# Performance work log

Measured on AMD Instinct MI355X. Metric: run time of the kernel, lower is better.

The kernel has to match this reference:

```python
import jax, jax.numpy as jnp
import numpy as np

HEADS = 4  # from init_kwargs

def setup_inputs() -> dict:
    key = jax.random.key(0)
    ks = jax.random.split(key, 11)
    B, N, T, E = 1, 16, 2048, 64
    D = E // HEADS
    return {
        "value": jax.random.normal(ks[0], (B, N, T, E), jnp.float32),
        "key":   jax.random.normal(ks[1], (B, N, T, E), jnp.float32),
        "query": jax.random.normal(ks[2], (B, N, T, E), jnp.float32),
        "Wq": jax.random.normal(ks[3], (D, D), jnp.float32) / np.sqrt(D),
        "bq": jax.random.normal(ks[4], (D,), jnp.float32) * 0.01,
        "Wk": jax.random.normal(ks[5], (D, D), jnp.float32) / np.sqrt(D),
        "bk": jax.random.normal(ks[6], (D,), jnp.float32) * 0.01,
        "Wv": jax.random.normal(ks[7], (D, D), jnp.float32) / np.sqrt(D),
        "bv": jax.random.normal(ks[8], (D,), jnp.float32) * 0.01,
        "Wfc": jax.random.normal(ks[9], (E, E), jnp.float32) / np.sqrt(E),
        "bfc": jax.random.normal(ks[10], (E,), jnp.float32) * 0.01,
    }

def reference(value, key, query, Wq, bq, Wk, bk, Wv, bv, Wfc, bfc):
    B, N, T, E = query.shape
    H = HEADS
    D = E // H
    # split heads: [B,N,T,H,D]
    q = query.reshape(B, N, T, H, D) @ Wq + bq
    k = key.reshape(B, N, T, H, D) @ Wk + bk
    v = value.reshape(B, N, T, H, D) @ Wv + bv
    # full score tensor [B,N,Tq,Tk,H]
    scores = jnp.einsum('bnqhd,bnkhd->bnqkh', q, k)
    # NOTE: original softmaxes over dim=2, i.e. the QUERY axis (faithful to source)
    attn = jax.nn.softmax(scores / jnp.float32(E) ** 0.5, axis=2)
    out = jnp.einsum('bnqkh,bnkhd->bnqhd', attn, v).reshape(B, N, T, E)
    return out @ Wfc + bfc
```

## Files before the change

kernel.cpp:

```cpp
#include <hip/hip_runtime.h>

#define N_ 16
#define T_ 2048
#define E_ 64
#define H_ 4
#define D_ 16
#define NH_ 64
#define SEXP_ 0.18033688f

typedef __attribute__((ext_vector_type(4))) _Float16 h4;
typedef __attribute__((ext_vector_type(8))) _Float16 h8;
typedef __attribute__((ext_vector_type(2))) __fp16 g2;
typedef __attribute__((ext_vector_type(4))) float f4;

#if __has_builtin(__builtin_amdgcn_exp2f)
__device__ inline float fast_exp2(float x) { return __builtin_amdgcn_exp2f(x); }
#else
__device__ inline float fast_exp2(float x) {
    float r; asm("v_exp_f32 %0, %1" : "=v"(r) : "v"(x)); return r;
}
#endif

#if __has_builtin(__builtin_amdgcn_rcpf)
__device__ inline float fast_rcp(float x) { return __builtin_amdgcn_rcpf(x); }
#else
__device__ inline float fast_rcp(float x) {
    float r; asm("v_rcp_f32 %0, %1" : "=v"(r) : "v"(x)); return r;
}
#endif

__device__ inline h4 pack4_f16(float a, float b, float c, float d) {
    union { g2 g[2]; h4 h; } u;
    u.g[0] = __builtin_amdgcn_cvt_pkrtz(a, b);
    u.g[1] = __builtin_amdgcn_cvt_pkrtz(c, d);
    return u.h;
}

__global__ __launch_bounds__(256) void proj_kernel(
    const float* __restrict__ xq, const float* __restrict__ Wq, const float* __restrict__ bq,
    const float* __restrict__ xk, const float* __restrict__ Wk, const float* __restrict__ bk,
    const float* __restrict__ xv, const float* __restrict__ Wv, const float* __restrict__ bv,
    const float* __restrict__ Wfc,
    _Float16* __restrict__ Qh, _Float16* __restrict__ Kh, _Float16* __restrict__ Vt,
    _Float16* __restrict__ Wt)
{
    int tid = threadIdx.x;
    int y = blockIdx.y;
    if (y == 3) {
        if (blockIdx.x < 16) {
            int k = blockIdx.x * 4 + (tid >> 6);
            int e = tid & 63;
            Wt[e * 64 + k] = (_Float16)Wfc[k * 64 + e];
        }
        return;
    }
    const float* x = (y == 0) ? xq : (y == 1) ? xk : xv;
    const float* W = (y == 0) ? Wq : (y == 1) ? Wk : Wv;
    const float* b = (y == 0) ? bq : (y == 1) ? bk : bv;
    const float sc = (y == 0) ? SEXP_ : 1.0f;

    __shared__ float Wl[D_ * D_];
    __shared__ float bl[D_];
    Wl[tid] = W[tid];
    if (tid < D_) bl[tid] = b[tid];
    __syncthreads();

    int r = blockIdx.x * 256 + tid;
    int h, t, n;
    if (y == 2) {
        t = r & (T_ - 1);
        h = (r >> 11) & (H_ - 1);
        n = r >> 13;
    } else {
        h = r & (H_ - 1);
        t = (r >> 2) & (T_ - 1);
        n = r >> 13;
    }

    const float4* xp4 = reinterpret_cast<const float4*>(
        x + ((size_t)(n * T_ + t) * E_ + h * D_));
    float xv_[D_];
#pragma unroll
    for (int i = 0; i < 4; i++) {
        float4 v = xp4[i];
        xv_[4*i] = v.x; xv_[4*i+1] = v.y; xv_[4*i+2] = v.z; xv_[4*i+3] = v.w;
    }
    float acc[D_];
#pragma unroll
    for (int i = 0; i < D_; i++) acc[i] = bl[i];
#pragma unroll
    for (int j = 0; j < D_; j++) {
        float xj = xv_[j];
#pragma unroll
        for (int i = 0; i < D_; i++) acc[i] = fmaf(xj, Wl[j * D_ + i], acc[i]);
    }
    if (y == 2) {
        _Float16* vb = Vt + (size_t)(n * H_ + h) * D_ * T_ + t;
#pragma unroll
        for (int d = 0; d < D_; d++) vb[(size_t)d * T_] = (_Float16)acc[d];
    } else {
        _Float16 ob[16];
#pragma unroll
        for (int i = 0; i < D_; i++) ob[i] = (_Float16)(acc[i] * sc);
        _Float16* o = (y == 0) ? Qh : Kh;
        uint4* dst = reinterpret_cast<uint4*>(o + (size_t)((n * H_ + h) * T_ + t) * D_);
        dst[0] = reinterpret_cast<uint4*>(ob)[0];
        dst[1] = reinterpret_cast<uint4*>(ob)[1];
    }
}

#define S_PHASE(PD) do {                                                      \
    lp = (f4){0.f, 0.f, 0.f, 0.f};                                            \
    _Pragma("unroll")                                                         \
    for (int j = 0; j < 8; j++) {                                             \
        h4 bj = *reinterpret_cast<const h4*>(QsW + (j * 16 + row) * 20 + quad * 4); \
        f4 s = __builtin_amdgcn_mfma_f32_16x16x16f16(a, bj, z4, 0, 0, 0);     \
        float e0 = fast_exp2(s[0]), e1 = fast_exp2(s[1]);                     \
        float e2 = fast_exp2(s[2]), e3 = fast_exp2(s[3]);                     \
        lp[0] += e0; lp[1] += e1; lp[2] += e2; lp[3] += e3;                   \
        PD[j] = pack4_f16(e0, e1, e2, e3);                                    \
    }                                                                         \
} while (0)

#define SWZ_STEP(M)                                                           \
    lp[0] += __int_as_float(__builtin_amdgcn_ds_swizzle(__float_as_int(lp[0]), M)); \
    lp[1] += __int_as_float(__builtin_amdgcn_ds_swizzle(__float_as_int(lp[1]), M)); \
    lp[2] += __int_as_float(__builtin_amdgcn_ds_swizzle(__float_as_int(lp[2]), M)); \
    lp[3] += __int_as_float(__builtin_amdgcn_ds_swizzle(__float_as_int(lp[3]), M));

#define REDUCE(BDST) do {                                                     \
    SWZ_STEP(0x041F) SWZ_STEP(0x081F) SWZ_STEP(0x101F) SWZ_STEP(0x201F)       \
    if (row == 0) {                                                           \
        _Pragma("unroll")                                                     \
        for (int i = 0; i < 4; i++) atomicAdd(&l[BDST][quad * 4 + i], lp[i]); \
    }                                                                         \
} while (0)

#define ITER(C, PS, PPV, KN) do {                                             \
    int k0 = k_lo + (C) * 16;                                                 \
    h4 v = *reinterpret_cast<const h4*>(Vb + (k0 - 16) + quad * 4);           \
    f4 la = *reinterpret_cast<f4*>(&l[bm1][quad * 4]);                        \
    S_PHASE(PS);                                                              \
    h4 na = *reinterpret_cast<const h4*>(Kb + ((KN) + row) * D_ + quad * 4);  \
    REDUCE(b0);                                                               \
    {                                                                         \
        union { g2 g[2]; h4 h; } u_;                                          \
        u_.g[0] = __builtin_amdgcn_cvt_pkrtz(fast_rcp(la[0]), fast_rcp(la[1])); \
        u_.g[1] = __builtin_amdgcn_cvt_pkrtz(fast_rcp(la[2]), fast_rcp(la[3])); \
        v = v * u_.h;                                                         \
    }                                                                         \
    _Pragma("unroll")                                                         \
    for (int j = 0; j < 8; j++)                                               \
        o[j] = __builtin_amdgcn_mfma_f32_16x16x16f16(PPV[j], v, o[j], 0, 0, 0); \
    if (wave == 0 && lane < 16) l[bp1][lane] = 0.f;                           \
    __syncthreads();                                                          \
    a = na;                                                                   \
} while (0)

#define ROT() do { int t_ = bm1; bm1 = b0; b0 = bp1; bp1 = t_; } while (0)

__global__ __attribute__((amdgpu_flat_work_group_size(1024, 1024)))
           __attribute__((amdgpu_waves_per_eu(4, 4)))
void fused_attn_kernel(
    const _Float16* __restrict__ Qh, const _Float16* __restrict__ Kh,
    const _Float16* __restrict__ Vt, float* __restrict__ PO)
{
    __shared__ __align__(16) _Float16 Qs[16 * 128 * 20];
    __shared__ __align__(16) float l[3][16];
    int tid = threadIdx.x;
    int lane = tid & 63, wave = tid >> 6;
    int row = lane & 15, quad = lane >> 4;
    int nh = blockIdx.x;
    int z = blockIdx.y;
    int k_lo = z * (T_ / 4);

    const _Float16* Kb = Kh + (size_t)nh * T_ * D_;
    const _Float16* Qb = Qh + (size_t)nh * T_ * D_;
    const _Float16* Vb = Vt + (size_t)nh * D_ * T_ + (size_t)row * T_;

    if (tid < 48) ((float*)l)[tid] = 0.f;

    {
        const uint2* src = reinterpret_cast<const uint2*>(Qb);
        uint2* dq = reinterpret_cast<uint2*>(Qs);
#pragma unroll
        for (int s = 0; s < 8; s++) {
            int u = s * 1024 + tid;
            dq[(u >> 2) * 5 + (u & 3)] = src[u];
        }
    }
    const _Float16* QsW = Qs + wave * (128 * 20);

    f4 o[8];
#pragma unroll
    for (int j = 0; j < 8; j++) o[j] = (f4){0.f, 0.f, 0.f, 0.f};
    f4 z4 = {0.f, 0.f, 0.f, 0.f};

    h4 a = *reinterpret_cast<const h4*>(Kb + (k_lo + row) * D_ + quad * 4);
    h4 pA[8], pB[8];
    f4 lp;

    __syncthreads();

    S_PHASE(pA);
    {
        h4 na = *reinterpret_cast<const h4*>(Kb + (k_lo + 16 + row) * D_ + quad * 4);
        REDUCE(0);
        __syncthreads();
        a = na;
    }

    int bm1 = 0, b0 = 1, bp1 = 2;
#pragma unroll 1
    for (int c = 1; c < 31; c += 2) {
        ITER(c,     pB, pA, k_lo + c * 16 + 16);
        ROT();
        ITER(c + 1, pA, pB, k_lo + c * 16 + 32);
        ROT();
    }
    ITER(31, pB, pA, k_lo);
    ROT();

    {
        h4 v = *reinterpret_cast<const h4*>(Vb + (k_lo + 31 * 16) + quad * 4);
        f4 la = *reinterpret_cast<f4*>(&l[bm1][quad * 4]);
        union { g2 g[2]; h4 h; } u_;
        u_.g[0] = __builtin_amdgcn_cvt_pkrtz(fast_rcp(la[0]), fast_rcp(la[1]));
        u_.g[1] = __builtin_amdgcn_cvt_pkrtz(fast_rcp(la[2]), fast_rcp(la[3]));
        v = v * u_.h;
#pragma unroll
        for (int j = 0; j < 8; j++)
            o[j] = __builtin_amdgcn_mfma_f32_16x16x16f16(pB[j], v, o[j], 0, 0, 0);
    }

    int n = nh >> 2, h = nh & 3;
    float* po = PO + (size_t)z * N_ * T_ * E_ + (size_t)n * T_ * E_ + h * D_ + row;
#pragma unroll
    for (int j = 0; j < 8; j++)
#pragma unroll
        for (int i = 0; i < 4; i++) {
            int q0 = (wave * 8 + j) * 16 + quad * 4 + i;
            po[(size_t)q0 * E_] = o[j][i];
        }
}

__global__ __launch_bounds__(256) void fc_kernel(
    const float* __restrict__ PO, const _Float16* __restrict__ Wt,
    const float* __restrict__ bfc, float* __restrict__ out)
{
    int tid = threadIdx.x;
    int lane = tid & 63, wave = tid >> 6;
    int row = lane & 15, quad = lane >> 4;
    int g = blockIdx.x * 4 + wave;
    int r0 = g * 16;
    size_t base = (size_t)(r0 + row) * E_;
    const size_t zstride = (size_t)N_ * T_ * E_ / 4;

    h8 a[2];
#pragma unroll
    for (int half = 0; half < 2; half++) {
        f4 u0 = {0.f,0.f,0.f,0.f}, u1 = {0.f,0.f,0.f,0.f};
#pragma unroll
        for (int zz = 0; zz < 4; zz++) {
            const f4* p = reinterpret_cast<const f4*>(PO) + zz * zstride + base / 4;
            f4 w0 = p[half * 8 + quad * 2];
            f4 w1 = p[half * 8 + quad * 2 + 1];
#pragma unroll
            for (int i = 0; i < 4; i++) { u0[i] += w0[i]; u1[i] += w1[i]; }
        }
        union { h4 h[2]; h8 v; } pk;
        pk.h[0] = pack4_f16(u0[0], u0[1], u0[2], u0[3]);
        pk.h[1] = pack4_f16(u1[0], u1[1], u1[2], u1[3]);
        a[half] = pk.v;
    }
    f4 acc[4];
#pragma unroll
    for (int ne = 0; ne < 4; ne++) {
        const _Float16* wtb = Wt + (size_t)(ne * 16 + row) * 64;
        h8 b0 = *reinterpret_cast<const h8*>(wtb + quad * 8);
        h8 b1 = *reinterpret_cast<const h8*>(wtb + 32 + quad * 8);
        acc[ne] = __builtin_amdgcn_mfma_f32_16x16x32_f16(a[0], b0, (f4){0.f,0.f,0.f,0.f}, 0, 0, 0);
        acc[ne] = __builtin_amdgcn_mfma_f32_16x16x32_f16(a[1], b1, acc[ne], 0, 0, 0);
    }
#pragma unroll
    for (int ne = 0; ne < 4; ne++) {
        float bias = bfc[ne * 16 + row];
#pragma unroll
        for (int i = 0; i < 4; i++)
            out[(size_t)(r0 + quad * 4 + i) * E_ + ne * 16 + row] = acc[ne][i] + bias;
    }
}

extern "C" void kernel_launch(void* const* d_in, const int* in_sizes, int n_in,
                              void* d_out, int out_size, void* d_ws, size_t ws_size,
                              hipStream_t stream) {
    (void)in_sizes; (void)n_in; (void)out_size; (void)ws_size;
    const float* value = (const float*)d_in[0];
    const float* key   = (const float*)d_in[1];
    const float* query = (const float*)d_in[2];
    const float* Wq    = (const float*)d_in[3];
    const float* bq    = (const float*)d_in[4];
    const float* Wk    = (const float*)d_in[5];
    const float* bk    = (const float*)d_in[6];
    const float* Wv    = (const float*)d_in[7];
    const float* bv    = (const float*)d_in[8];
    const float* Wfc   = (const float*)d_in[9];
    const float* bfc   = (const float*)d_in[10];
    float* out = (float*)d_out;

    char* ws = (char*)d_ws;
    _Float16* Qh  = (_Float16*)(ws);
    _Float16* Kh  = (_Float16*)(ws + (4u << 20));
    _Float16* Vt  = (_Float16*)(ws + (8u << 20));
    _Float16* Wt  = (_Float16*)(ws + (12u << 20));
    float*    PO  = (float*)   (ws + (15u << 20));

    proj_kernel<<<dim3(512, 4), 256, 0, stream>>>(
        query, Wq, bq, key, Wk, bk, value, Wv, bv, Wfc, Qh, Kh, Vt, Wt);
    fused_attn_kernel<<<dim3(NH_, 4), 1024, 0, stream>>>(Qh, Kh, Vt, PO);
    fc_kernel<<<512, 256, 0, stream>>>(PO, Wt, bfc, out);
}
```

Before: 163.6 us.

## Fuse output projection into attention kernel using atomic accumulation

Removes the separate fc kernel and the fp32 partial-output buffer. Each attention block now stages its per-head output in shared memory as fp16, multiplies it by its slice of Wfc with MFMA, and atomically adds into the final output. The output is zeroed beforehand by an extra grid row in the projection kernel. This trades a kernel launch and a large write-then-read of partial results for many fp32 atomics (16 contributions per output element) and non-deterministic summation order.

```diff
diff --git a/kernel.cpp b/kernel.cpp
--- a/kernel.cpp
+++ b/kernel.cpp
@@ -42,10 +42,18 @@
     const float* __restrict__ xv, const float* __restrict__ Wv, const float* __restrict__ bv,
     const float* __restrict__ Wfc,
     _Float16* __restrict__ Qh, _Float16* __restrict__ Kh, _Float16* __restrict__ Vt,
-    _Float16* __restrict__ Wt)
+    _Float16* __restrict__ Wt, float* __restrict__ outz)
 {
     int tid = threadIdx.x;
     int y = blockIdx.y;
+    if (y == 4) {
+        float4 zz = {0.f, 0.f, 0.f, 0.f};
+        float4* o4 = reinterpret_cast<float4*>(outz);
+        int tp = blockIdx.x * 256 + tid;
+#pragma unroll
+        for (int s = 0; s < 4; s++) o4[tp + s * 131072] = zz;
+        return;
+    }
     if (y == 3) {
         if (blockIdx.x < 16) {
             int k = blockIdx.x * 4 + (tid >> 6);
@@ -163,7 +171,8 @@
            __attribute__((amdgpu_waves_per_eu(4, 4)))
 void fused_attn_kernel(
     const _Float16* __restrict__ Qh, const _Float16* __restrict__ Kh,
-    const _Float16* __restrict__ Vt, float* __restrict__ PO)
+    const _Float16* __restrict__ Vt, const _Float16* __restrict__ Wt,
+    const float* __restrict__ bfc, float* __restrict__ out)
 {
     __shared__ __align__(16) _Float16 Qs[16 * 128 * 20];
     __shared__ __align__(16) float l[3][16];
@@ -233,61 +242,40 @@
             o[j] = __builtin_amdgcn_mfma_f32_16x16x16f16(pB[j], v, o[j], 0, 0, 0);
     }
 
+    _Float16* Tw = Qs + wave * (128 * 20);
+#pragma unroll
+    for (int j = 0; j < 8; j++)
+        *reinterpret_cast<h4*>(Tw + j * 256 + row * 16 + quad * 4) =
+            pack4_f16(o[j][0], o[j][1], o[j][2], o[j][3]);
+    asm volatile("s_waitcnt lgkmcnt(0)" ::: "memory");
+    __builtin_amdgcn_sched_barrier(0);
+
     int n = nh >> 2, h = nh & 3;
-    float* po = PO + (size_t)z * N_ * T_ * E_ + (size_t)n * T_ * E_ + h * D_ + row;
-#pragma unroll
-    for (int j = 0; j < 8; j++)
-#pragma unroll
-        for (int i = 0; i < 4; i++) {
-            int q0 = (wave * 8 + j) * 16 + quad * 4 + i;
-            po[(size_t)q0 * E_] = o[j][i];
+    h4 wf[4];
+    float bb[4];
+#pragma unroll
+    for (int ne = 0; ne < 4; ne++) {
+        wf[ne] = *reinterpret_cast<const h4*>(
+            Wt + (size_t)(ne * 16 + row) * 64 + h * 16 + quad * 4);
+        bb[ne] = bfc[ne * 16 + row] * 0.0625f;
+    }
+    float* ob = out + (size_t)n * T_ * E_;
+#pragma unroll
+    for (int j = 0; j < 8; j++) {
+        _Float16 r0 = Tw[j * 256 + (quad * 4 + 0) * 16 + row];
+        _Float16 r1 = Tw[j * 256 + (quad * 4 + 1) * 16 + row];
+        _Float16 r2 = Tw[j * 256 + (quad * 4 + 2) * 16 + row];
+        _Float16 r3 = Tw[j * 256 + (quad * 4 + 3) * 16 + row];
+        h4 af = (h4){r0, r1, r2, r3};
+        int q0 = (wave * 8 + j) * 16;
+#pragma unroll
+        for (int ne = 0; ne < 4; ne++) {
+            f4 acc = __builtin_amdgcn_mfma_f32_16x16x16f16(af, wf[ne], z4, 0, 0, 0);
+#pragma unroll
+            for (int ii = 0; ii < 4; ii++)
+                atomicAdd(ob + (size_t)(q0 + quad * 4 + ii) * E_ + ne * 16 + row,
+                          acc[ii] + bb[ne]);
         }
-}
-
-__global__ __launch_bounds__(256) void fc_kernel(
-    const float* __restrict__ PO, const _Float16* __restrict__ Wt,
-    const float* __restrict__ bfc, float* __restrict__ out)
-{
-    int tid = threadIdx.x;
-    int lane = tid & 63, wave = tid >> 6;
-    int row = lane & 15, quad = lane >> 4;
-    int g = blockIdx.x * 4 + wave;
-    int r0 = g * 16;
-    size_t base = (size_t)(r0 + row) * E_;
-    const size_t zstride = (size_t)N_ * T_ * E_ / 4;
-
-    h8 a[2];
-#pragma unroll
-    for (int half = 0; half < 2; half++) {
-        f4 u0 = {0.f,0.f,0.f,0.f}, u1 = {0.f,0.f,0.f,0.f};
-#pragma unroll
-        for (int zz = 0; zz < 4; zz++) {
-            const f4* p = reinterpret_cast<const f4*>(PO) + zz * zstride + base / 4;
-            f4 w0 = p[half * 8 + quad * 2];
-            f4 w1 = p[half * 8 + quad * 2 + 1];
-#pragma unroll
-            for (int i = 0; i < 4; i++) { u0[i] += w0[i]; u1[i] += w1[i]; }
-        }
-        union { h4 h[2]; h8 v; } pk;
-        pk.h[0] = pack4_f16(u0[0], u0[1], u0[2], u0[3]);
-        pk.h[1] = pack4_f16(u1[0], u1[1], u1[2], u1[3]);
-        a[half] = pk.v;
-    }
-    f4 acc[4];
-#pragma unroll
-    for (int ne = 0; ne < 4; ne++) {
-        const _Float16* wtb = Wt + (size_t)(ne * 16 + row) * 64;
-        h8 b0 = *reinterpret_cast<const h8*>(wtb + quad * 8);
-        h8 b1 = *reinterpret_cast<const h8*>(wtb + 32 + quad * 8);
-        acc[ne] = __builtin_amdgcn_mfma_f32_16x16x32_f16(a[0], b0, (f4){0.f,0.f,0.f,0.f}, 0, 0, 0);
-        acc[ne] = __builtin_amdgcn_mfma_f32_16x16x32_f16(a[1], b1, acc[ne], 0, 0, 0);
-    }
-#pragma unroll
-    for (int ne = 0; ne < 4; ne++) {
-        float bias = bfc[ne * 16 + row];
-#pragma unroll
-        for (int i = 0; i < 4; i++)
-            out[(size_t)(r0 + quad * 4 + i) * E_ + ne * 16 + row] = acc[ne][i] + bias;
     }
 }
 
@@ -313,10 +301,8 @@
     _Float16* Kh  = (_Float16*)(ws + (4u << 20));
     _Float16* Vt  = (_Float16*)(ws + (8u << 20));
     _Float16* Wt  = (_Float16*)(ws + (12u << 20));
-    float*    PO  = (float*)   (ws + (15u << 20));
-
-    proj_kernel<<<dim3(512, 4), 256, 0, stream>>>(
-        query, Wq, bq, key, Wk, bk, value, Wv, bv, Wfc, Qh, Kh, Vt, Wt);
-    fused_attn_kernel<<<dim3(NH_, 4), 1024, 0, stream>>>(Qh, Kh, Vt, PO);
-    fc_kernel<<<512, 256, 0, stream>>>(PO, Wt, bfc, out);
-}
+
+    proj_kernel<<<dim3(512, 5), 256, 0, stream>>>(
+        query, Wq, bq, key, Wk, bk, value, Wv, bv, Wfc, Qh, Kh, Vt, Wt, out);
+    fused_attn_kernel<<<dim3(NH_, 4), 1024, 0, stream>>>(Qh, Kh, Vt, Wt, bfc, out);
+}
```

After: 250.8 us. 1.53x slower.
